# Performance work log

Measured on AMD Instinct MI355X. Metric: run time of the kernel, lower is better.

## Reference

```python
import jax, jax.numpy as jnp
import numpy as np

NUM_HEADS = 16
HIDDEN = 1024
HEAD_DIM = HIDDEN // NUM_HEADS


def setup_inputs() -> dict:
    key = jax.random.key(0)
    ks = jax.random.split(key, 8)
    B, S, H = 4, 2048, HIDDEN
    scale = 1.0 / np.sqrt(H)
    return {
        "hidden_states": jax.random.normal(ks[0], (B, S, H), dtype=jnp.float32),
        "attention_mask": jnp.zeros((B, S), dtype=jnp.float32),
        "Wq": jax.random.normal(ks[1], (H, H), dtype=jnp.float32) * scale,
        "bq": jnp.zeros((H,), dtype=jnp.float32),
        "Wk": jax.random.normal(ks[2], (H, H), dtype=jnp.float32) * scale,
        "bk": jnp.zeros((H,), dtype=jnp.float32),
        "Wv": jax.random.normal(ks[3], (H, H), dtype=jnp.float32) * scale,
        "bv": jnp.zeros((H,), dtype=jnp.float32),
    }


def reference(hidden_states, attention_mask, Wq, bq, Wk, bk, Wv, bv):
    B, S, H = hidden_states.shape
    nh, hd = NUM_HEADS, HEAD_DIM
    # Linear projections (torch Linear: x @ W.T + b)
    q = hidden_states @ Wq.T + bq
    k = hidden_states @ Wk.T + bk
    v = hidden_states @ Wv.T + bv
    # [B, S, H] -> [B, nh, S, hd]
    q = q.reshape(B, S, nh, hd).transpose(0, 2, 1, 3)
    k = k.reshape(B, S, nh, hd).transpose(0, 2, 1, 3)
    v = v.reshape(B, S, nh, hd).transpose(0, 2, 1, 3)
    # Scores [B, nh, S, S]
    scores = jnp.einsum("bhqd,bhkd->bhqk", q, k) / jnp.sqrt(jnp.float32(hd))
    # Additive mask broadcast [B, 1, 1, S]
    scores = scores + attention_mask[:, None, None, :]
    probs = jax.nn.softmax(scores, axis=-1)
    # Dropout prob = 0.0 (eval): identity
    context = jnp.einsum("bhqk,bhkd->bhqd", probs, v)
    # [B, nh, S, hd] -> [B, S, H]
    return context.transpose(0, 2, 1, 3).reshape(B, S, H)
```

## Files before the change

kernel.cpp:

```cpp
#include <hip/hip_runtime.h>
#include <hip/hip_bf16.h>
#include <stdint.h>

#define NH 16
#define HD 64
#define H_ 1024
#define S_ 2048
#define B_ 4
#define MROWS 8192

typedef __attribute__((ext_vector_type(4))) float f32x4;
typedef __attribute__((ext_vector_type(8))) short s16x8;

__device__ __forceinline__ unsigned short f2bf(float x) {
  unsigned int u = __float_as_uint(x);
  u += 0x7fffu + ((u >> 16) & 1u);
  return (unsigned short)(u >> 16);
}
__device__ __forceinline__ unsigned int pack_bf2(float lo, float hi) {
  return (unsigned int)f2bf(lo) | ((unsigned int)f2bf(hi) << 16);
}

__device__ __forceinline__ void ld_lds16(void* lds, const void* g) {
  __builtin_amdgcn_global_load_lds(
      (const __attribute__((address_space(1))) unsigned int*)g,
      (__attribute__((address_space(3))) unsigned int*)lds, 16, 0, 0);
}

__global__ void cvt_bf16_k(const float* __restrict__ src,
                           unsigned short* __restrict__ dst, int n4) {
  int i = blockIdx.x * blockDim.x + threadIdx.x;
  if (i >= n4) return;
  float4 v = reinterpret_cast<const float4*>(src)[i];
  ushort4 o;
  o.x = f2bf(v.x); o.y = f2bf(v.y); o.z = f2bf(v.z); o.w = f2bf(v.w);
  reinterpret_cast<ushort4*>(dst)[i] = o;
}

__global__ __launch_bounds__(256) void qkv_gemm_k(
    const unsigned short* __restrict__ Xb,
    const unsigned short* __restrict__ Wb,
    const float* __restrict__ bq, const float* __restrict__ bk,
    const float* __restrict__ bv,
    unsigned short* __restrict__ outAll) {
  __shared__ unsigned short As[128 * 32];
  __shared__ unsigned short Bs[128 * 32];
  int z = blockIdx.z;
  const unsigned short* Wp = Wb + (size_t)z * (H_ * H_);
  const float* bias = (z == 0) ? bq : (z == 1) ? bk : bv;
  unsigned short* outp = outAll + (size_t)z * ((size_t)MROWS * H_);
  int m0 = blockIdx.y * 128, n0 = blockIdx.x * 128;
  int tid = threadIdx.x;
  int w = tid >> 6, l = tid & 63;
  int wr = w >> 1, wc = w & 1;
  int g = l >> 4, ln = l & 15;
  f32x4 acc[4][4] = {};
  for (int k0 = 0; k0 < H_; k0 += 32) {
    __syncthreads();
#pragma unroll
    for (int a = 0; a < 2; ++a) {
      int ci = (w * 2 + a) * 64 + l;
      int row = ci >> 2, c = ci & 3;
      ld_lds16(&As[(w * 2 + a) * 512], &Xb[(size_t)(m0 + row) * H_ + k0 + c * 8]);
      ld_lds16(&Bs[(w * 2 + a) * 512], &Wp[(size_t)(n0 + row) * H_ + k0 + c * 8]);
    }
    __syncthreads();
    s16x8 aF[4], bF[4];
#pragma unroll
    for (int mi = 0; mi < 4; ++mi)
      aF[mi] = *reinterpret_cast<const s16x8*>(&As[(wr * 64 + mi * 16 + ln) * 32 + 8 * g]);
#pragma unroll
    for (int ni = 0; ni < 4; ++ni)
      bF[ni] = *reinterpret_cast<const s16x8*>(&Bs[(wc * 64 + ni * 16 + ln) * 32 + 8 * g]);
#pragma unroll
    for (int mi = 0; mi < 4; ++mi)
#pragma unroll
      for (int ni = 0; ni < 4; ++ni)
        acc[mi][ni] = __builtin_amdgcn_mfma_f32_16x16x32_bf16(aF[mi], bF[ni], acc[mi][ni], 0, 0, 0);
  }
#pragma unroll
  for (int ni = 0; ni < 4; ++ni) {
    int ncol = n0 + wc * 64 + ni * 16 + ln;
    float bvv = bias[ncol];
    int h = ncol >> 6, d = ncol & 63;
#pragma unroll
    for (int mi = 0; mi < 4; ++mi) {
#pragma unroll
      for (int j = 0; j < 4; ++j) {
        int m = m0 + wr * 64 + mi * 16 + 4 * g + j;
        int b = m >> 11, s = m & 2047;
        outp[((size_t)((b << 4) + h) * S_ + s) * HD + d] = f2bf(acc[mi][ni][j] + bvv);
      }
    }
  }
}

__global__ __launch_bounds__(256) void attn_k(
    const unsigned short* __restrict__ Qh, const unsigned short* __restrict__ Kh,
    const unsigned short* __restrict__ Vh, const float* __restrict__ mask,
    float* __restrict__ out) {
  __shared__ unsigned short Ks[64 * 72];
  __shared__ unsigned short Vt[64 * 72];
  __shared__ unsigned short Pl[4 * 16 * 72];
  __shared__ float maskS[64];
  int bh = blockIdx.y;
  int b = bh >> 4, h = bh & 15;
  int tid = threadIdx.x;
  int w = tid >> 6, l = tid & 63;
  int g = l >> 4, ln = l & 15;
  int qbase = blockIdx.x * 64 + w * 16;
  const unsigned short* Qp = Qh + ((size_t)bh * S_ + qbase + ln) * HD;
  s16x8 qf[2];
  qf[0] = *reinterpret_cast<const s16x8*>(Qp + 8 * g);
  qf[1] = *reinterpret_cast<const s16x8*>(Qp + 32 + 8 * g);
  float m_run = -INFINITY, l_run = 0.0f;
  f32x4 ctx[4] = {};
  unsigned short* Pw = &Pl[w * 16 * 72];
  const size_t kvbase = (size_t)bh * S_ * HD;

  for (int k0 = 0; k0 < S_; k0 += 64) {
    __syncthreads();
#pragma unroll
    for (int a = 0; a < 2; ++a) {
      int c = tid + a * 256;
      int row = c >> 3, cc = c & 7;
      s16x8 kv = *reinterpret_cast<const s16x8*>(&Kh[kvbase + (size_t)(k0 + row) * HD + cc * 8]);
      *reinterpret_cast<s16x8*>(&Ks[row * 72 + cc * 8]) = kv;
      s16x8 vv = *reinterpret_cast<const s16x8*>(&Vh[kvbase + (size_t)(k0 + row) * HD + cc * 8]);
#pragma unroll
      for (int j = 0; j < 8; ++j)
        Vt[(cc * 8 + j) * 72 + row] = (unsigned short)vv[j];
    }
    if (tid < 64) maskS[tid] = mask[b * S_ + k0 + tid];
    __syncthreads();

    f32x4 sacc[4] = {};
#pragma unroll
    for (int ks = 0; ks < 2; ++ks) {
#pragma unroll
      for (int mt = 0; mt < 4; ++mt) {
        s16x8 kf = *reinterpret_cast<const s16x8*>(&Ks[(mt * 16 + ln) * 72 + ks * 32 + 8 * g]);
        sacc[mt] = __builtin_amdgcn_mfma_f32_16x16x32_bf16(kf, qf[ks], sacc[mt], 0, 0, 0);
      }
    }
    float p[4][4];
    float mymax = -INFINITY;
#pragma unroll
    for (int mt = 0; mt < 4; ++mt)
#pragma unroll
      for (int r = 0; r < 4; ++r) {
        float v = sacc[mt][r] * 0.125f + maskS[mt * 16 + 4 * g + r];
        p[mt][r] = v;
        mymax = fmaxf(mymax, v);
      }
    mymax = fmaxf(mymax, __shfl_xor(mymax, 16));
    mymax = fmaxf(mymax, __shfl_xor(mymax, 32));
    float m_new = fmaxf(m_run, mymax);
    float alpha = __expf(m_run - m_new);
    float sum = 0.0f;
#pragma unroll
    for (int mt = 0; mt < 4; ++mt)
#pragma unroll
      for (int r = 0; r < 4; ++r) {
        float e = __expf(p[mt][r] - m_new);
        p[mt][r] = e;
        sum += e;
      }
    sum += __shfl_xor(sum, 16);
    sum += __shfl_xor(sum, 32);
    l_run = l_run * alpha + sum;
    m_run = m_new;
#pragma unroll
    for (int mt = 0; mt < 4; ++mt)
#pragma unroll
      for (int rp = 0; rp < 2; ++rp)
        *reinterpret_cast<unsigned int*>(&Pw[ln * 72 + mt * 16 + 4 * g + 2 * rp]) =
            pack_bf2(p[mt][2 * rp], p[mt][2 * rp + 1]);
    float resc[4];
#pragma unroll
    for (int r = 0; r < 4; ++r)
      resc[r] = __shfl(alpha, (l & 48) + 4 * g + r);
#pragma unroll
    for (int nt = 0; nt < 4; ++nt)
#pragma unroll
      for (int r = 0; r < 4; ++r) ctx[nt][r] *= resc[r];
#pragma unroll
    for (int ks = 0; ks < 2; ++ks) {
      s16x8 pa = *reinterpret_cast<const s16x8*>(&Pw[ln * 72 + ks * 32 + 8 * g]);
#pragma unroll
      for (int nt = 0; nt < 4; ++nt) {
        s16x8 vf = *reinterpret_cast<const s16x8*>(&Vt[(nt * 16 + ln) * 72 + ks * 32 + 8 * g]);
        ctx[nt] = __builtin_amdgcn_mfma_f32_16x16x32_bf16(pa, vf, ctx[nt], 0, 0, 0);
      }
    }
  }
  float inv[4];
#pragma unroll
  for (int r = 0; r < 4; ++r)
    inv[r] = 1.0f / __shfl(l_run, (l & 48) + 4 * g + r);
#pragma unroll
  for (int nt = 0; nt < 4; ++nt) {
#pragma unroll
    for (int r = 0; r < 4; ++r) {
      int q = qbase + 4 * g + r;
      out[((size_t)(b * S_ + q)) * H_ + h * HD + nt * 16 + ln] = ctx[nt][r] * inv[r];
    }
  }
}

extern "C" void kernel_launch(void* const* d_in, const int* in_sizes, int n_in,
                              void* d_out, int out_size, void* d_ws, size_t ws_size,
                              hipStream_t stream) {
  (void)in_sizes; (void)n_in; (void)out_size; (void)ws_size;
  const float* hs = (const float*)d_in[0];
  const float* mask = (const float*)d_in[1];
  const float* Wq = (const float*)d_in[2];
  const float* bq = (const float*)d_in[3];
  const float* Wk = (const float*)d_in[4];
  const float* bk = (const float*)d_in[5];
  const float* Wv = (const float*)d_in[6];
  const float* bv = (const float*)d_in[7];
  float* out = (float*)d_out;

  unsigned short* Xb = (unsigned short*)d_ws;
  unsigned short* Wb = Xb + (size_t)MROWS * H_;
  unsigned short* QKVh = Wb + (size_t)3 * H_ * H_;

  cvt_bf16_k<<<(MROWS * H_ / 4 + 255) / 256, 256, 0, stream>>>(hs, Xb, MROWS * H_ / 4);
  cvt_bf16_k<<<(H_ * H_ / 4 + 255) / 256, 256, 0, stream>>>(Wq, Wb, H_ * H_ / 4);
  cvt_bf16_k<<<(H_ * H_ / 4 + 255) / 256, 256, 0, stream>>>(Wk, Wb + H_ * H_, H_ * H_ / 4);
  cvt_bf16_k<<<(H_ * H_ / 4 + 255) / 256, 256, 0, stream>>>(Wv, Wb + 2 * H_ * H_, H_ * H_ / 4);

  qkv_gemm_k<<<dim3(8, 64, 3), 256, 0, stream>>>(Xb, Wb, bq, bk, bv, QKVh);

  attn_k<<<dim3(32, 64), 256, 0, stream>>>(QKVh, QKVh + (size_t)MROWS * H_,
                                           QKVh + (size_t)2 * MROWS * H_, mask, out);
}
```

Baseline: 417.7 us.

## Store V pre-transposed from QKV GEMM and register-prefetch next K/V tile

The projection GEMM now writes V in [b,h,d,s] layout, so the attention kernel can copy V tiles into shared memory with 16-byte vector stores instead of scalar transposing stores. The attention loop also loads the next K/V tile into registers while the current tile is being computed, hiding global load latency. The cost is scattered 2-byte global stores for V in the GEMM epilogue, which coalesce worse, plus extra register pressure in the attention kernel.

```diff
diff --git a/kernel.cpp b/kernel.cpp
--- a/kernel.cpp
+++ b/kernel.cpp
@@ -89,7 +89,11 @@
       for (int j = 0; j < 4; ++j) {
         int m = m0 + wr * 64 + mi * 16 + 4 * g + j;
         int b = m >> 11, s = m & 2047;
-        outp[((size_t)((b << 4) + h) * S_ + s) * HD + d] = f2bf(acc[mi][ni][j] + bvv);
+        unsigned short val = f2bf(acc[mi][ni][j] + bvv);
+        if (z == 2)
+          outp[((size_t)((b << 4) + h) * HD + d) * S_ + s] = val;
+        else
+          outp[((size_t)((b << 4) + h) * S_ + s) * HD + d] = val;
       }
     }
   }
@@ -97,10 +101,10 @@
 
 __global__ __launch_bounds__(256) void attn_k(
     const unsigned short* __restrict__ Qh, const unsigned short* __restrict__ Kh,
-    const unsigned short* __restrict__ Vh, const float* __restrict__ mask,
+    const unsigned short* __restrict__ Vtg, const float* __restrict__ mask,
     float* __restrict__ out) {
   __shared__ unsigned short Ks[64 * 72];
-  __shared__ unsigned short Vt[64 * 72];
+  __shared__ unsigned short Vs[64 * 72];
   __shared__ unsigned short Pl[4 * 16 * 72];
   __shared__ float maskS[64];
   int bh = blockIdx.y;
@@ -118,20 +122,29 @@
   unsigned short* Pw = &Pl[w * 16 * 72];
   const size_t kvbase = (size_t)bh * S_ * HD;
 
+  int r0 = tid >> 3, c0 = tid & 7;
+  int r1 = r0 + 32;
+  s16x8 kreg[2], vreg[2];
+  {
+    kreg[0] = *reinterpret_cast<const s16x8*>(&Kh[kvbase + (size_t)r0 * HD + c0 * 8]);
+    kreg[1] = *reinterpret_cast<const s16x8*>(&Kh[kvbase + (size_t)r1 * HD + c0 * 8]);
+    vreg[0] = *reinterpret_cast<const s16x8*>(&Vtg[kvbase + (size_t)r0 * S_ + c0 * 8]);
+    vreg[1] = *reinterpret_cast<const s16x8*>(&Vtg[kvbase + (size_t)r1 * S_ + c0 * 8]);
+  }
+
   for (int k0 = 0; k0 < S_; k0 += 64) {
     __syncthreads();
-#pragma unroll
-    for (int a = 0; a < 2; ++a) {
-      int c = tid + a * 256;
-      int row = c >> 3, cc = c & 7;
-      s16x8 kv = *reinterpret_cast<const s16x8*>(&Kh[kvbase + (size_t)(k0 + row) * HD + cc * 8]);
-      *reinterpret_cast<s16x8*>(&Ks[row * 72 + cc * 8]) = kv;
-      s16x8 vv = *reinterpret_cast<const s16x8*>(&Vh[kvbase + (size_t)(k0 + row) * HD + cc * 8]);
-#pragma unroll
-      for (int j = 0; j < 8; ++j)
-        Vt[(cc * 8 + j) * 72 + row] = (unsigned short)vv[j];
-    }
+    *reinterpret_cast<s16x8*>(&Ks[r0 * 72 + c0 * 8]) = kreg[0];
+    *reinterpret_cast<s16x8*>(&Ks[r1 * 72 + c0 * 8]) = kreg[1];
+    *reinterpret_cast<s16x8*>(&Vs[r0 * 72 + c0 * 8]) = vreg[0];
+    *reinterpret_cast<s16x8*>(&Vs[r1 * 72 + c0 * 8]) = vreg[1];
     if (tid < 64) maskS[tid] = mask[b * S_ + k0 + tid];
+    if (k0 + 64 < S_) {
+      kreg[0] = *reinterpret_cast<const s16x8*>(&Kh[kvbase + (size_t)(k0 + 64 + r0) * HD + c0 * 8]);
+      kreg[1] = *reinterpret_cast<const s16x8*>(&Kh[kvbase + (size_t)(k0 + 64 + r1) * HD + c0 * 8]);
+      vreg[0] = *reinterpret_cast<const s16x8*>(&Vtg[kvbase + (size_t)r0 * S_ + k0 + 64 + c0 * 8]);
+      vreg[1] = *reinterpret_cast<const s16x8*>(&Vtg[kvbase + (size_t)r1 * S_ + k0 + 64 + c0 * 8]);
+    }
     __syncthreads();
 
     f32x4 sacc[4] = {};
@@ -189,7 +202,7 @@
       s16x8 pa = *reinterpret_cast<const s16x8*>(&Pw[ln * 72 + ks * 32 + 8 * g]);
 #pragma unroll
       for (int nt = 0; nt < 4; ++nt) {
-        s16x8 vf = *reinterpret_cast<const s16x8*>(&Vt[(nt * 16 + ln) * 72 + ks * 32 + 8 * g]);
+        s16x8 vf = *reinterpret_cast<const s16x8*>(&Vs[(nt * 16 + ln) * 72 + ks * 32 + 8 * g]);
         ctx[nt] = __builtin_amdgcn_mfma_f32_16x16x32_bf16(pa, vf, ctx[nt], 0, 0, 0);
       }
     }
```

After: 348.6 us. 16.6% less time.
